# Kernel optimization log

Hardware: AMD Instinct MI355X
Metric: run time of the kernel (lower is better)

Reference implementation:

```python
import jax, jax.numpy as jnp
import numpy as np

THETA = 40.0


def setup_inputs() -> dict:
    key = jax.random.key(0)
    k1, k2 = jax.random.split(key)
    B, C, H, W = 4, 19, 192, 192
    mask = jax.random.normal(k1, (B, C, H, W), dtype=jnp.float32)
    edge = jax.random.uniform(k2, (B, 1, H, W), dtype=jnp.float32)
    return {"mask": mask, "edge": edge, "iter": 3}


def _criss_cross_attention(edge):
    # edge: [B,1,H,W] -> attention logits over K = H + W - 1 criss-cross positions
    e = jax.nn.relu(edge)
    max_edge = e.max()
    hc = jnp.cumsum(e, axis=2)[:, 0]  # [B,H,W] column integral image
    wc = jnp.cumsum(e, axis=3)[:, 0]  # [B,H,W] row integral image
    B, H, W = hc.shape
    # column part: weight[b,t,i,j] = |hc[b,t,j] - hc[b,i,j]|, t in [0,H)
    w_col = jnp.abs(hc[:, :, None, :] - hc[:, None, :, :])  # [B,H,H,W] (b,t,i,j)
    # row part over all columns s: |wc[b,i,s] - wc[b,i,j]|
    wct = wc.transpose(0, 2, 1)  # [B,W(s),H(i)]
    w_row_full = jnp.abs(wct[:, :, :, None] - wc[:, None, :, :])  # [B,W,H,W] (b,s,i,j)
    # drop s == j (self column, already counted in column part): W-1 entries
    t = jnp.arange(W - 1)[:, None]
    j = jnp.arange(W)[None, :]
    idx = t + (t >= j).astype(t.dtype)  # [W-1, W]: source column for slot t at pixel column j
    w_row = jnp.take_along_axis(w_row_full, idx[None, :, None, :], axis=1)  # [B,W-1,H,W]
    logits = -THETA * (jnp.concatenate([w_col, w_row], axis=1) - max_edge)  # [B,H+W-1,H,W]
    attn = jax.nn.softmax(logits, axis=1)
    a_col = attn[:, :H]  # [B,H,H,W]
    a_row = attn[:, H:]  # [B,W-1,H,W]
    # scatter row attention back to full [B,W,H,W] (zero at s==j) for a dense einsum
    attn_full = jnp.zeros((B, W, H, W), attn.dtype).at[:, idx, :, j].set(
        a_row.transpose(1, 3, 0, 2)
    )
    return a_col, attn_full


def reference(mask, edge, iter):
    a_col, a_row_full = _criss_cross_attention(edge)
    feat = mask  # [B,C,H,W]
    for _ in range(iter):
        out_c = jnp.einsum('btij,bctj->bcij', a_col, feat)       # column gather
        out_r = jnp.einsum('bsij,bcis->bcij', a_row_full, feat)  # row gather
        feat = out_c + out_r
    return feat
```

## Files before the change

### kernel.cpp

```cpp
#include <hip/hip_runtime.h>

#define B 4
#define C 19
#define H 192
#define W 192
#define HW (H * W)
#define THETA_LOG2E 57.70780163555855f

#define CSEGS 8
#define CSR 24
#define NCOLB (B * C * 3)
#define NROWB (B * C * H / 8)
#define NTHR 512

__device__ __forceinline__ unsigned short f2b(float x) {
    unsigned u = __float_as_uint(x);
    u = (u + 0x7FFFu + ((u >> 16) & 1u)) >> 16;
    return (unsigned short)u;
}
__device__ __forceinline__ float b2f(unsigned short h) {
    return __uint_as_float(((unsigned)h) << 16);
}

template<bool FIRST>
__global__ __launch_bounds__(NTHR) void k_iter(const float* __restrict__ mask,
                                               const float* __restrict__ edge,
                                               const unsigned short* __restrict__ csin,
                                               const unsigned short* __restrict__ rsin,
                                               unsigned short* __restrict__ csout,
                                               unsigned short* __restrict__ rsout,
                                               float* __restrict__ dcol,
                                               float* __restrict__ drow) {
    const int t = threadIdx.x;
    if (blockIdx.x < NCOLB) {
        __shared__ float sPf[CSEGS * 64], sQf[CSEGS * 64], sPb[CSEGS * 64], sQb[CSEGS * 64];
        int blk = blockIdx.x;
        int jt = blk % 3, bc = blk / 3, b = bc / C, c = bc % C;
        int jl = t & 63, seg = t >> 6;
        int j = jt * 64 + jl, i0 = seg * CSR;

        const float* ep = edge + ((size_t)b * H + i0) * W + j;
        const size_t fb = ((size_t)bc * H + i0) * W + j;
        const size_t db = ((size_t)b * H + i0) * W + j;

        float dr[CSR + 1], fr[CSR];
        #pragma unroll
        for (int r = 0; r < CSR; ++r) dr[r] = exp2f(-THETA_LOG2E * fmaxf(ep[r * W], 0.f));
        dr[CSR] = (seg < CSEGS - 1) ? exp2f(-THETA_LOG2E * fmaxf(ep[CSR * W], 0.f)) : 0.f;

        if (FIRST) {
            #pragma unroll
            for (int r = 0; r < CSR; ++r) fr[r] = mask[fb + r * W];
        } else {
            #pragma unroll
            for (int r = 0; r < CSR; ++r) {
                float cs = b2f(csin[fb + r * W]);
                float rs = b2f(rsin[fb + r * W]);
                float rd = 1.f / (dcol[db + r * W] + drow[db + r * W] - 1.f);
                fr[r] = (cs + rs) * rd;
            }
        }

        float Pf = 1.f, Qf = 0.f, Pb = 1.f, Qb = 0.f;
        #pragma unroll
        for (int r = 0; r < CSR; ++r) { Qf = Qf * dr[r] + fr[r]; Pf *= dr[r]; }
        #pragma unroll
        for (int r = CSR - 1; r >= 0; --r) { Qb = Qb * dr[r + 1] + fr[r]; Pb *= dr[r + 1]; }
        sPf[seg * 64 + jl] = Pf; sQf[seg * 64 + jl] = Qf;
        sPb[seg * 64 + jl] = Pb; sQb[seg * 64 + jl] = Qb;
        __syncthreads();
        if (seg == 0) {
            float P = sPf[jl], Q = sQf[jl];
            for (int s2 = 1; s2 < CSEGS; ++s2) {
                float Pc = sPf[s2 * 64 + jl], Qc = sQf[s2 * 64 + jl];
                Q = Q * Pc + Qc; P = P * Pc;
                sPf[s2 * 64 + jl] = P; sQf[s2 * 64 + jl] = Q;
            }
        } else if (seg == 1) {
            float P = sPb[(CSEGS - 1) * 64 + jl], Q = sQb[(CSEGS - 1) * 64 + jl];
            for (int s2 = CSEGS - 2; s2 >= 0; --s2) {
                float Pc = sPb[s2 * 64 + jl], Qc = sQb[s2 * 64 + jl];
                Q = Q * Pc + Qc; P = P * Pc;
                sPb[s2 * 64 + jl] = P; sQb[s2 * 64 + jl] = Q;
            }
        }
        __syncthreads();
        float z = (seg > 0) ? sQf[(seg - 1) * 64 + jl] : 0.f;
        float s = (seg < CSEGS - 1) ? sQb[(seg + 1) * 64 + jl] : 0.f;
        float zarr[CSR];
        #pragma unroll
        for (int r = 0; r < CSR; ++r) { z = z * dr[r] + fr[r]; zarr[r] = z; }
        #pragma unroll
        for (int r = CSR - 1; r >= 0; --r) {
            s = s * dr[r + 1] + fr[r];
            csout[fb + r * W] = f2b(zarr[r] + s - fr[r]);
        }

        if (FIRST && c == 0) {
            float Pf2 = 1.f, Qf2 = 0.f, Pb2 = 1.f, Qb2 = 0.f;
            #pragma unroll
            for (int r = 0; r < CSR; ++r) { Qf2 = Qf2 * dr[r] + 1.f; Pf2 *= dr[r]; }
            #pragma unroll
            for (int r = CSR - 1; r >= 0; --r) { Qb2 = Qb2 * dr[r + 1] + 1.f; Pb2 *= dr[r + 1]; }
            __syncthreads();
            sPf[seg * 64 + jl] = Pf2; sQf[seg * 64 + jl] = Qf2;
            sPb[seg * 64 + jl] = Pb2; sQb[seg * 64 + jl] = Qb2;
            __syncthreads();
            if (seg == 0) {
                float P = sPf[jl], Q = sQf[jl];
                for (int s2 = 1; s2 < CSEGS; ++s2) {
                    float Pc = sPf[s2 * 64 + jl], Qc = sQf[s2 * 64 + jl];
                    Q = Q * Pc + Qc; P = P * Pc;
                    sPf[s2 * 64 + jl] = P; sQf[s2 * 64 + jl] = Q;
                }
            } else if (seg == 1) {
                float P = sPb[(CSEGS - 1) * 64 + jl], Q = sQb[(CSEGS - 1) * 64 + jl];
                for (int s2 = CSEGS - 2; s2 >= 0; --s2) {
                    float Pc = sPb[s2 * 64 + jl], Qc = sQb[s2 * 64 + jl];
                    Q = Q * Pc + Qc; P = P * Pc;
                    sPb[s2 * 64 + jl] = P; sQb[s2 * 64 + jl] = Q;
                }
            }
            __syncthreads();
            float zu = (seg > 0) ? sQf[(seg - 1) * 64 + jl] : 0.f;
            float su = (seg < CSEGS - 1) ? sQb[(seg + 1) * 64 + jl] : 0.f;
            #pragma unroll
            for (int r = 0; r < CSR; ++r) { zu = zu * dr[r] + 1.f; zarr[r] = zu; }
            #pragma unroll
            for (int r = CSR - 1; r >= 0; --r) {
                su = su * dr[r + 1] + 1.f;
                dcol[db + r * W] = zarr[r] + su - 1.f;
            }
        }
    } else {
        int rblk = blockIdx.x - NCOLB;
        int wave = t >> 6, lane = t & 63;
        int rr = rblk * 8 + wave;
        int i = rr % H;
        int c = (rr / H) % C;
        int b = rr / (H * C);
        const size_t rb = ((size_t)(b * C + c) * H + i) * W;
        const int db = (b * H + i) * W;
        const int s0 = 3 * lane;

        float e0 = edge[db + s0], e1 = edge[db + s0 + 1], e2 = edge[db + s0 + 2];
        float d0 = exp2f(-THETA_LOG2E * fmaxf(e0, 0.f));
        float d1 = exp2f(-THETA_LOG2E * fmaxf(e1, 0.f));
        float d2 = exp2f(-THETA_LOG2E * fmaxf(e2, 0.f));
        float d3 = 0.f;
        if (lane < 63) {
            float e3 = edge[db + s0 + 3];
            d3 = exp2f(-THETA_LOG2E * fmaxf(e3, 0.f));
        }

        float f0, f1, f2;
        if (FIRST) {
            f0 = mask[rb + s0]; f1 = mask[rb + s0 + 1]; f2 = mask[rb + s0 + 2];
        } else {
            float rd0 = 1.f / (dcol[db + s0]     + drow[db + s0]     - 1.f);
            float rd1 = 1.f / (dcol[db + s0 + 1] + drow[db + s0 + 1] - 1.f);
            float rd2 = 1.f / (dcol[db + s0 + 2] + drow[db + s0 + 2] - 1.f);
            f0 = (b2f(csin[rb + s0])     + b2f(rsin[rb + s0]))     * rd0;
            f1 = (b2f(csin[rb + s0 + 1]) + b2f(rsin[rb + s0 + 1])) * rd1;
            f2 = (b2f(csin[rb + s0 + 2]) + b2f(rsin[rb + s0 + 2])) * rd2;
        }

        float P = d0 * d1 * d2;
        float Q = (f0 * d1 + f1) * d2 + f2;
        #pragma unroll
        for (int off = 1; off < 64; off <<= 1) {
            float Pp = __shfl_up(P, off);
            float Qp = __shfl_up(Q, off);
            if (lane >= off) { Q = Qp * P + Q; P = Pp * P; }
        }
        float zin = __shfl_up(Q, 1);
        if (lane == 0) zin = 0.f;
        float zA = zin * d0 + f0;
        float zB = zA * d1 + f1;
        float zC = zB * d2 + f2;

        float Pb = d3 * d2 * d1;
        float Qb = (f2 * d2 + f1) * d1 + f0;
        #pragma unroll
        for (int off = 1; off < 64; off <<= 1) {
            float Pp = __shfl_down(Pb, off);
            float Qp = __shfl_down(Qb, off);
            if (lane < 64 - off) { Qb = Qp * Pb + Qb; Pb = Pp * Pb; }
        }
        float sin_ = __shfl_down(Qb, 1);
        if (lane == 63) sin_ = 0.f;
        float sC = sin_ * d3 + f2;
        float sB = sC * d2 + f1;
        float sA = sB * d1 + f0;

        rsout[rb + s0]     = f2b(zA + sA - 2.f * f0);
        rsout[rb + s0 + 1] = f2b(zB + sB - 2.f * f1);
        rsout[rb + s0 + 2] = f2b(zC + sC - 2.f * f2);

        if (FIRST && c == 0) {
            float Pu = d0 * d1 * d2;
            float Qu = d1 * d2 + d2 + 1.f;
            #pragma unroll
            for (int off = 1; off < 64; off <<= 1) {
                float Pp = __shfl_up(Pu, off);
                float Qp = __shfl_up(Qu, off);
                if (lane >= off) { Qu = Qp * Pu + Qu; Pu = Pp * Pu; }
            }
            float zuin = __shfl_up(Qu, 1);
            if (lane == 0) zuin = 0.f;
            float zuA = zuin * d0 + 1.f;
            float zuB = zuA * d1 + 1.f;
            float zuC = zuB * d2 + 1.f;

            float Pub = d3 * d2 * d1;
            float Qub = d2 * d1 + d1 + 1.f;
            #pragma unroll
            for (int off = 1; off < 64; off <<= 1) {
                float Pp = __shfl_down(Pub, off);
                float Qp = __shfl_down(Qub, off);
                if (lane < 64 - off) { Qub = Qp * Pub + Qub; Pub = Pp * Pub; }
            }
            float suin = __shfl_down(Qub, 1);
            if (lane == 63) suin = 0.f;
            float suC = suin * d3 + 1.f;
            float suB = suC * d2 + 1.f;
            float suA = suB * d1 + 1.f;

            drow[db + s0]     = zuA + suA - 1.f;
            drow[db + s0 + 1] = zuB + suB - 1.f;
            drow[db + s0 + 2] = zuC + suC - 1.f;
        }
    }
}

__global__ __launch_bounds__(256) void k_comb(const unsigned short* __restrict__ cs,
                                              const unsigned short* __restrict__ rs,
                                              const float* __restrict__ dcol,
                                              const float* __restrict__ drow,
                                              float* __restrict__ out) {
    int idx4 = (blockIdx.x * 256 + threadIdx.x) * 4;
    int bc = idx4 / HW;
    int rem = idx4 - bc * HW;
    int b = bc / C;
    size_t db = (size_t)b * HW + rem;
    uint2 csu = *(const uint2*)(cs + idx4);
    uint2 rsu = *(const uint2*)(rs + idx4);
    float4 dc = *(const float4*)(dcol + db);
    float4 dw = *(const float4*)(drow + db);
    float4 o;
    o.x = (b2f((unsigned short)(csu.x & 0xffff)) + b2f((unsigned short)(rsu.x & 0xffff))) / (dc.x + dw.x - 1.f);
    o.y = (b2f((unsigned short)(csu.x >> 16))    + b2f((unsigned short)(rsu.x >> 16)))    / (dc.y + dw.y - 1.f);
    o.z = (b2f((unsigned short)(csu.y & 0xffff)) + b2f((unsigned short)(rsu.y & 0xffff))) / (dc.z + dw.z - 1.f);
    o.w = (b2f((unsigned short)(csu.y >> 16))    + b2f((unsigned short)(rsu.y >> 16)))    / (dc.w + dw.w - 1.f);
    *(float4*)(out + idx4) = o;
}

extern "C" void kernel_launch(void* const* d_in, const int* in_sizes, int n_in,
                              void* d_out, int out_size, void* d_ws, size_t ws_size,
                              hipStream_t stream) {
    const float* mask = (const float*)d_in[0];
    const float* edge = (const float*)d_in[1];
    float* out = (float*)d_out;

    float* dcol = (float*)d_ws;
    float* drow = dcol + (size_t)B * HW;
    unsigned short* csA = (unsigned short*)(drow + (size_t)B * HW);
    unsigned short* rsA = csA + (size_t)B * C * HW;
    unsigned short* csB = rsA + (size_t)B * C * HW;
    unsigned short* rsB = csB + (size_t)B * C * HW;

    const int grid = NCOLB + NROWB;

    k_iter<true><<<grid, NTHR, 0, stream>>>(mask, edge, nullptr, nullptr, csA, rsA, dcol, drow);
    k_iter<false><<<grid, NTHR, 0, stream>>>(nullptr, edge, csA, rsA, csB, rsB, dcol, drow);
    k_iter<false><<<grid, NTHR, 0, stream>>>(nullptr, edge, csB, rsB, csA, rsA, dcol, drow);
    k_comb<<<(B * C * HW) / (4 * 256), 256, 0, stream>>>(csA, rsA, dcol, drow, out);
}
```

Baseline: 50.91 us.

## Cache reciprocal normaliser across iterations and double block size

The second iteration now stores the reciprocal of the normaliser (dcol + drow - 1), written once per batch by the c==0 column blocks. The third iteration and the combine kernel read that single cached array instead of loading dcol and drow and dividing, which removes one float stream and a divide per pixel on those paths. Separately, column segments grow from 8 to 16, with 12 rows each, and blocks go from 512 to 1024 threads, with the row branch handling 16 rows per block. The larger blocks trade a shorter per-thread serial scan for a longer cross-segment scan and possibly lower scheduling flexibility.

```diff
diff --git a/kernel.cpp b/kernel.cpp
--- a/kernel.cpp
+++ b/kernel.cpp
@@ -7,11 +7,11 @@
 #define HW (H * W)
 #define THETA_LOG2E 57.70780163555855f
 
-#define CSEGS 8
-#define CSR 24
+#define CSEGS 16
+#define CSR 12
 #define NCOLB (B * C * 3)
-#define NROWB (B * C * H / 8)
-#define NTHR 512
+#define NROWB (B * C * H / 16)
+#define NTHR 1024
 
 __device__ __forceinline__ unsigned short f2b(float x) {
     unsigned u = __float_as_uint(x);
@@ -22,7 +22,7 @@
     return __uint_as_float(((unsigned)h) << 16);
 }
 
-template<bool FIRST>
+template<int MODE>
 __global__ __launch_bounds__(NTHR) void k_iter(const float* __restrict__ mask,
                                                const float* __restrict__ edge,
                                                const unsigned short* __restrict__ csin,
@@ -30,7 +30,8 @@
                                                unsigned short* __restrict__ csout,
                                                unsigned short* __restrict__ rsout,
                                                float* __restrict__ dcol,
-                                               float* __restrict__ drow) {
+                                               float* __restrict__ drow,
+                                               float* __restrict__ rDg) {
     const int t = threadIdx.x;
     if (blockIdx.x < NCOLB) {
         __shared__ float sPf[CSEGS * 64], sQf[CSEGS * 64], sPb[CSEGS * 64], sQb[CSEGS * 64];
@@ -48,16 +49,24 @@
         for (int r = 0; r < CSR; ++r) dr[r] = exp2f(-THETA_LOG2E * fmaxf(ep[r * W], 0.f));
         dr[CSR] = (seg < CSEGS - 1) ? exp2f(-THETA_LOG2E * fmaxf(ep[CSR * W], 0.f)) : 0.f;
 
-        if (FIRST) {
+        if (MODE == 0) {
             #pragma unroll
             for (int r = 0; r < CSR; ++r) fr[r] = mask[fb + r * W];
-        } else {
+        } else if (MODE == 1) {
             #pragma unroll
             for (int r = 0; r < CSR; ++r) {
                 float cs = b2f(csin[fb + r * W]);
                 float rs = b2f(rsin[fb + r * W]);
                 float rd = 1.f / (dcol[db + r * W] + drow[db + r * W] - 1.f);
                 fr[r] = (cs + rs) * rd;
+                if (c == 0) rDg[db + r * W] = rd;
+            }
+        } else {
+            #pragma unroll
+            for (int r = 0; r < CSR; ++r) {
+                float cs = b2f(csin[fb + r * W]);
+                float rs = b2f(rsin[fb + r * W]);
+                fr[r] = (cs + rs) * rDg[db + r * W];
             }
         }
 
@@ -96,7 +105,7 @@
             csout[fb + r * W] = f2b(zarr[r] + s - fr[r]);
         }
 
-        if (FIRST && c == 0) {
+        if (MODE == 0 && c == 0) {
             float Pf2 = 1.f, Qf2 = 0.f, Pb2 = 1.f, Qb2 = 0.f;
             #pragma unroll
             for (int r = 0; r < CSR; ++r) { Qf2 = Qf2 * dr[r] + 1.f; Pf2 *= dr[r]; }
@@ -135,7 +144,7 @@
     } else {
         int rblk = blockIdx.x - NCOLB;
         int wave = t >> 6, lane = t & 63;
-        int rr = rblk * 8 + wave;
+        int rr = rblk * 16 + wave;
         int i = rr % H;
         int c = (rr / H) % C;
         int b = rr / (H * C);
@@ -154,15 +163,19 @@
         }
 
         float f0, f1, f2;
-        if (FIRST) {
+        if (MODE == 0) {
             f0 = mask[rb + s0]; f1 = mask[rb + s0 + 1]; f2 = mask[rb + s0 + 2];
-        } else {
+        } else if (MODE == 1) {
             float rd0 = 1.f / (dcol[db + s0]     + drow[db + s0]     - 1.f);
             float rd1 = 1.f / (dcol[db + s0 + 1] + drow[db + s0 + 1] - 1.f);
             float rd2 = 1.f / (dcol[db + s0 + 2] + drow[db + s0 + 2] - 1.f);
             f0 = (b2f(csin[rb + s0])     + b2f(rsin[rb + s0]))     * rd0;
             f1 = (b2f(csin[rb + s0 + 1]) + b2f(rsin[rb + s0 + 1])) * rd1;
             f2 = (b2f(csin[rb + s0 + 2]) + b2f(rsin[rb + s0 + 2])) * rd2;
+        } else {
+            f0 = (b2f(csin[rb + s0])     + b2f(rsin[rb + s0]))     * rDg[db + s0];
+            f1 = (b2f(csin[rb + s0 + 1]) + b2f(rsin[rb + s0 + 1])) * rDg[db + s0 + 1];
+            f2 = (b2f(csin[rb + s0 + 2]) + b2f(rsin[rb + s0 + 2])) * rDg[db + s0 + 2];
         }
 
         float P = d0 * d1 * d2;
@@ -197,7 +210,7 @@
         rsout[rb + s0 + 1] = f2b(zB + sB - 2.f * f1);
         rsout[rb + s0 + 2] = f2b(zC + sC - 2.f * f2);
 
-        if (FIRST && c == 0) {
+        if (MODE == 0 && c == 0) {
             float Pu = d0 * d1 * d2;
             float Qu = d1 * d2 + d2 + 1.f;
             #pragma unroll
@@ -235,8 +248,7 @@
 
 __global__ __launch_bounds__(256) void k_comb(const unsigned short* __restrict__ cs,
                                               const unsigned short* __restrict__ rs,
-                                              const float* __restrict__ dcol,
-                                              const float* __restrict__ drow,
+                                              const float* __restrict__ rDg,
                                               float* __restrict__ out) {
     int idx4 = (blockIdx.x * 256 + threadIdx.x) * 4;
     int bc = idx4 / HW;
@@ -245,13 +257,12 @@
     size_t db = (size_t)b * HW + rem;
     uint2 csu = *(const uint2*)(cs + idx4);
     uint2 rsu = *(const uint2*)(rs + idx4);
-    float4 dc = *(const float4*)(dcol + db);
-    float4 dw = *(const float4*)(drow + db);
+    float4 rd = *(const float4*)(rDg + db);
     float4 o;
-    o.x = (b2f((unsigned short)(csu.x & 0xffff)) + b2f((unsigned short)(rsu.x & 0xffff))) / (dc.x + dw.x - 1.f);
-    o.y = (b2f((unsigned short)(csu.x >> 16))    + b2f((unsigned short)(rsu.x >> 16)))    / (dc.y + dw.y - 1.f);
-    o.z = (b2f((unsigned short)(csu.y & 0xffff)) + b2f((unsigned short)(rsu.y & 0xffff))) / (dc.z + dw.z - 1.f);
-    o.w = (b2f((unsigned short)(csu.y >> 16))    + b2f((unsigned short)(rsu.y >> 16)))    / (dc.w + dw.w - 1.f);
+    o.x = (b2f((unsigned short)(csu.x & 0xffff)) + b2f((unsigned short)(rsu.x & 0xffff))) * rd.x;
+    o.y = (b2f((unsigned short)(csu.x >> 16))    + b2f((unsigned short)(rsu.x >> 16)))    * rd.y;
+    o.z = (b2f((unsigned short)(csu.y & 0xffff)) + b2f((unsigned short)(rsu.y & 0xffff))) * rd.z;
+    o.w = (b2f((unsigned short)(csu.y >> 16))    + b2f((unsigned short)(rsu.y >> 16)))    * rd.w;
     *(float4*)(out + idx4) = o;
 }
 
@@ -264,15 +275,16 @@
 
     float* dcol = (float*)d_ws;
     float* drow = dcol + (size_t)B * HW;
-    unsigned short* csA = (unsigned short*)(drow + (size_t)B * HW);
+    float* rDg  = drow + (size_t)B * HW;
+    unsigned short* csA = (unsigned short*)(rDg + (size_t)B * HW);
     unsigned short* rsA = csA + (size_t)B * C * HW;
     unsigned short* csB = rsA + (size_t)B * C * HW;
     unsigned short* rsB = csB + (size_t)B * C * HW;
 
     const int grid = NCOLB + NROWB;
 
-    k_iter<true><<<grid, NTHR, 0, stream>>>(mask, edge, nullptr, nullptr, csA, rsA, dcol, drow);
-    k_iter<false><<<grid, NTHR, 0, stream>>>(nullptr, edge, csA, rsA, csB, rsB, dcol, drow);
-    k_iter<false><<<grid, NTHR, 0, stream>>>(nullptr, edge, csB, rsB, csA, rsA, dcol, drow);
-    k_comb<<<(B * C * HW) / (4 * 256), 256, 0, stream>>>(csA, rsA, dcol, drow, out);
-}
+    k_iter<0><<<grid, NTHR, 0, stream>>>(mask, edge, nullptr, nullptr, csA, rsA, dcol, drow, nullptr);
+    k_iter<1><<<grid, NTHR, 0, stream>>>(nullptr, edge, csA, rsA, csB, rsB, dcol, drow, rDg);
+    k_iter<2><<<grid, NTHR, 0, stream>>>(nullptr, edge, csB, rsB, csA, rsA, nullptr, nullptr, rDg);
+    k_comb<<<(B * C * HW) / (4 * 256), 256, 0, stream>>>(csA, rsA, rDg, out);
+}
```

New measurement: 51.59 us. No clear change (+1.3%).

## Transpose column scans through shared memory and precompute transposed decay/denominator tables

Applied to the files above, without the earlier changes.

Column blocks now stage a full 192x64 tile of the column-sum input in LDS, then run each column as a single-wave shuffle-based linear-recurrence scan. This replaces the 8-segment register scan with its cross-segment shared-memory combine. The first kernel gets dedicated blocks that precompute transposed decay and normalizer tables (dT, dcolT, drowT) plus the normal-layout ones, so later iterations read them contiguously. Row blocks now each process two rows per wave. The change trades extra workspace and a larger LDS footprint, which may lower occupancy, for coalesced scans and less recomputation of exp2.

```diff
diff --git a/kernel.cpp b/kernel.cpp
--- a/kernel.cpp
+++ b/kernel.cpp
@@ -5,13 +5,17 @@
 #define H 192
 #define W 192
 #define HW (H * W)
+#define NP (B * C)
 #define THETA_LOG2E 57.70780163555855f
 
-#define CSEGS 8
-#define CSR 24
-#define NCOLB (B * C * 3)
-#define NROWB (B * C * H / 8)
-#define NTHR 512
+#define NCOL 228
+#define NROW 912
+#define RSTRIDE 7296
+
+#define C1_BEG (NCOL + NROW)
+#define C2_BEG (C1_BEG + 144)
+#define C3_BEG (C2_BEG + 12)
+#define NFIRST (C3_BEG + 12)
 
 __device__ __forceinline__ unsigned short f2b(float x) {
     unsigned u = __float_as_uint(x);
@@ -22,231 +26,271 @@
     return __uint_as_float(((unsigned)h) << 16);
 }
 
-template<bool FIRST>
-__global__ __launch_bounds__(NTHR) void k_iter(const float* __restrict__ mask,
+__device__ __forceinline__ void ks_scan(int lane, float f0, float f1, float f2v,
+                                        float d0, float d1, float d2, float d3,
+                                        float& zA, float& zB, float& zC,
+                                        float& sA, float& sB, float& sC) {
+    float P = d0 * d1 * d2;
+    float Q = (f0 * d1 + f1) * d2 + f2v;
+    #pragma unroll
+    for (int off = 1; off < 64; off <<= 1) {
+        float Pp = __shfl_up(P, off), Qp = __shfl_up(Q, off);
+        if (lane >= off) { Q = Qp * P + Q; P = Pp * P; }
+    }
+    float zin = __shfl_up(Q, 1);
+    if (lane == 0) zin = 0.f;
+    zA = zin * d0 + f0; zB = zA * d1 + f1; zC = zB * d2 + f2v;
+    float Pb = d3 * d2 * d1;
+    float Qb = (f2v * d2 + f1) * d1 + f0;
+    #pragma unroll
+    for (int off = 1; off < 64; off <<= 1) {
+        float Pp = __shfl_down(Pb, off), Qp = __shfl_down(Qb, off);
+        if (lane < 64 - off) { Qb = Qp * Pb + Qb; Pb = Pp * Pb; }
+    }
+    float sin_ = __shfl_down(Qb, 1);
+    if (lane == 63) sin_ = 0.f;
+    sC = sin_ * d3 + f2v; sB = sC * d2 + f1; sA = sB * d1 + f0;
+}
+
+__global__ __launch_bounds__(512) void k_first(const float* __restrict__ mask,
                                                const float* __restrict__ edge,
-                                               const unsigned short* __restrict__ csin,
+                                               unsigned short* __restrict__ csA,
+                                               unsigned short* __restrict__ rsA,
+                                               float* __restrict__ dT,
+                                               float* __restrict__ dcolN,
+                                               float* __restrict__ drowN,
+                                               float* __restrict__ dcolT,
+                                               float* __restrict__ drowT) {
+    __shared__ float tf[192 * 65];
+    __shared__ unsigned short tu[192 * 66];
+    const int t = threadIdx.x, lane = t & 63, wave = t >> 6;
+    const int bx = blockIdx.x;
+
+    if (bx < NCOL) {
+        int jt = bx % 3, p = bx / 3, b = p / C;
+        #pragma unroll
+        for (int k = 0; k < 12; ++k) {
+            int e = t + k * 512; int i = e >> 5, jp = e & 31;
+            float2 mv = *(const float2*)&mask[(size_t)p * HW + i * W + jt * 64 + 2 * jp];
+            ((unsigned*)tu)[33 * i + jp] = (unsigned)f2b(mv.x) | ((unsigned)f2b(mv.y) << 16);
+            float2 ev = *(const float2*)&edge[(size_t)b * HW + i * W + jt * 64 + 2 * jp];
+            tf[65 * i + 2 * jp]     = exp2f(-THETA_LOG2E * fmaxf(ev.x, 0.f));
+            tf[65 * i + 2 * jp + 1] = exp2f(-THETA_LOG2E * fmaxf(ev.y, 0.f));
+        }
+        __syncthreads();
+        #pragma unroll
+        for (int q = 0; q < 8; ++q) {
+            int jl = wave * 8 + q;
+            int r0 = 3 * lane;
+            float f0 = b2f(tu[r0 * 66 + jl]), f1 = b2f(tu[(r0 + 1) * 66 + jl]), f2v = b2f(tu[(r0 + 2) * 66 + jl]);
+            float d0 = tf[r0 * 65 + jl], d1 = tf[(r0 + 1) * 65 + jl], d2 = tf[(r0 + 2) * 65 + jl];
+            float d3 = (lane < 63) ? tf[(r0 + 3) * 65 + jl] : 0.f;
+            float zA, zB, zC, sA, sB, sC;
+            ks_scan(lane, f0, f1, f2v, d0, d1, d2, d3, zA, zB, zC, sA, sB, sC);
+            tu[r0 * 66 + jl]       = f2b(zA + sA - f0);
+            tu[(r0 + 1) * 66 + jl] = f2b(zB + sB - f1);
+            tu[(r0 + 2) * 66 + jl] = f2b(zC + sC - f2v);
+        }
+        __syncthreads();
+        #pragma unroll
+        for (int k = 0; k < 12; ++k) {
+            int e = t + k * 512; int i = e >> 5, jp = e & 31;
+            *(unsigned*)&csA[(size_t)p * HW + i * W + jt * 64 + 2 * jp] = ((unsigned*)tu)[33 * i + jp];
+        }
+    } else if (bx < NCOL + NROW) {
+        int rblk = bx - NCOL;
+        #pragma unroll
+        for (int k = 0; k < 2; ++k) {
+            int rr = rblk * 8 + wave + k * RSTRIDE;
+            int i = rr % H, c = (rr / H) % C, b = rr / (H * C);
+            size_t rb = (size_t)(b * C + c) * HW + (size_t)i * W;
+            size_t db = (size_t)b * HW + (size_t)i * W;
+            int s0 = 3 * lane;
+            float d0 = exp2f(-THETA_LOG2E * fmaxf(edge[db + s0], 0.f));
+            float d1 = exp2f(-THETA_LOG2E * fmaxf(edge[db + s0 + 1], 0.f));
+            float d2 = exp2f(-THETA_LOG2E * fmaxf(edge[db + s0 + 2], 0.f));
+            float d3 = 0.f;
+            if (lane < 63) d3 = exp2f(-THETA_LOG2E * fmaxf(edge[db + s0 + 3], 0.f));
+            float f0 = mask[rb + s0], f1 = mask[rb + s0 + 1], f2v = mask[rb + s0 + 2];
+            float zA, zB, zC, sA, sB, sC;
+            ks_scan(lane, f0, f1, f2v, d0, d1, d2, d3, zA, zB, zC, sA, sB, sC);
+            rsA[rb + s0]     = f2b(zA + sA - 2.f * f0);
+            rsA[rb + s0 + 1] = f2b(zB + sB - 2.f * f1);
+            rsA[rb + s0 + 2] = f2b(zC + sC - 2.f * f2v);
+        }
+    } else if (bx < C2_BEG) {
+        int blk = bx - C1_BEG;
+        int tx = blk % 6, ty = (blk / 6) % 6, b = blk / 36;
+        if (t < 256) {
+            int lx = t % 32, ly = t / 32;
+            #pragma unroll
+            for (int k = 0; k < 4; ++k) {
+                int il = ly + k * 8;
+                int I = ty * 32 + il, J = tx * 32 + lx;
+                float e = edge[(b * H + I) * W + J];
+                tf[il * 33 + lx] = exp2f(-THETA_LOG2E * fmaxf(e, 0.f));
+            }
+        }
+        __syncthreads();
+        if (t < 256) {
+            int lx = t % 32, ly = t / 32;
+            #pragma unroll
+            for (int k = 0; k < 4; ++k) {
+                int jl = ly + k * 8;
+                dT[((size_t)b * W + tx * 32 + jl) * H + ty * 32 + lx] = tf[lx * 33 + jl];
+            }
+        }
+    } else if (bx < C3_BEG) {
+        int bb = bx - C2_BEG; int jt = bb % 3, b = bb / 3;
+        #pragma unroll
+        for (int k = 0; k < 12; ++k) {
+            int e = t + k * 512; int i = e >> 5, jp = e & 31;
+            float2 ev = *(const float2*)&edge[(size_t)b * HW + i * W + jt * 64 + 2 * jp];
+            tf[65 * i + 2 * jp]     = exp2f(-THETA_LOG2E * fmaxf(ev.x, 0.f));
+            tf[65 * i + 2 * jp + 1] = exp2f(-THETA_LOG2E * fmaxf(ev.y, 0.f));
+        }
+        __syncthreads();
+        #pragma unroll
+        for (int q = 0; q < 8; ++q) {
+            int jl = wave * 8 + q;
+            int j = jt * 64 + jl;
+            int r0 = 3 * lane;
+            float d0 = tf[r0 * 65 + jl], d1 = tf[(r0 + 1) * 65 + jl], d2 = tf[(r0 + 2) * 65 + jl];
+            float d3 = (lane < 63) ? tf[(r0 + 3) * 65 + jl] : 0.f;
+            float zA, zB, zC, sA, sB, sC;
+            ks_scan(lane, 1.f, 1.f, 1.f, d0, d1, d2, d3, zA, zB, zC, sA, sB, sC);
+            float uA = zA + sA - 1.f, uB = zB + sB - 1.f, uC = zC + sC - 1.f;
+            size_t tb = ((size_t)b * W + j) * H + r0;
+            dcolT[tb] = uA; dcolT[tb + 1] = uB; dcolT[tb + 2] = uC;
+            tf[r0 * 65 + jl] = uA; tf[(r0 + 1) * 65 + jl] = uB; tf[(r0 + 2) * 65 + jl] = uC;
+        }
+        __syncthreads();
+        #pragma unroll
+        for (int k = 0; k < 24; ++k) {
+            int e = t + k * 512; int i = e >> 6, jl = e & 63;
+            dcolN[(size_t)b * HW + i * W + jt * 64 + jl] = tf[65 * i + jl];
+        }
+    } else {
+        int bb = bx - C3_BEG; int b = bb / 3, i0 = (bb % 3) * 64;
+        #pragma unroll
+        for (int k = 0; k < 8; ++k) {
+            int il = wave * 8 + k;
+            int i = i0 + il;
+            size_t db = (size_t)b * HW + (size_t)i * W;
+            int s0 = 3 * lane;
+            float d0 = exp2f(-THETA_LOG2E * fmaxf(edge[db + s0], 0.f));
+            float d1 = exp2f(-THETA_LOG2E * fmaxf(edge[db + s0 + 1], 0.f));
+            float d2 = exp2f(-THETA_LOG2E * fmaxf(edge[db + s0 + 2], 0.f));
+            float d3 = 0.f;
+            if (lane < 63) d3 = exp2f(-THETA_LOG2E * fmaxf(edge[db + s0 + 3], 0.f));
+            float zA, zB, zC, sA, sB, sC;
+            ks_scan(lane, 1.f, 1.f, 1.f, d0, d1, d2, d3, zA, zB, zC, sA, sB, sC);
+            float uA = zA + sA - 1.f, uB = zB + sB - 1.f, uC = zC + sC - 1.f;
+            drowN[db + s0] = uA; drowN[db + s0 + 1] = uB; drowN[db + s0 + 2] = uC;
+            tf[il * 193 + s0] = uA; tf[il * 193 + s0 + 1] = uB; tf[il * 193 + s0 + 2] = uC;
+        }
+        __syncthreads();
+        #pragma unroll
+        for (int k = 0; k < 24; ++k) {
+            int e = t + k * 512; int j = e >> 6, il = e & 63;
+            drowT[((size_t)b * W + j) * H + i0 + il] = tf[il * 193 + j];
+        }
+    }
+}
+
+__global__ __launch_bounds__(512) void k_iter2(const unsigned short* __restrict__ csin,
                                                const unsigned short* __restrict__ rsin,
                                                unsigned short* __restrict__ csout,
                                                unsigned short* __restrict__ rsout,
-                                               float* __restrict__ dcol,
-                                               float* __restrict__ drow) {
-    const int t = threadIdx.x;
-    if (blockIdx.x < NCOLB) {
-        __shared__ float sPf[CSEGS * 64], sQf[CSEGS * 64], sPb[CSEGS * 64], sQb[CSEGS * 64];
-        int blk = blockIdx.x;
-        int jt = blk % 3, bc = blk / 3, b = bc / C, c = bc % C;
-        int jl = t & 63, seg = t >> 6;
-        int j = jt * 64 + jl, i0 = seg * CSR;
-
-        const float* ep = edge + ((size_t)b * H + i0) * W + j;
-        const size_t fb = ((size_t)bc * H + i0) * W + j;
-        const size_t db = ((size_t)b * H + i0) * W + j;
-
-        float dr[CSR + 1], fr[CSR];
-        #pragma unroll
-        for (int r = 0; r < CSR; ++r) dr[r] = exp2f(-THETA_LOG2E * fmaxf(ep[r * W], 0.f));
-        dr[CSR] = (seg < CSEGS - 1) ? exp2f(-THETA_LOG2E * fmaxf(ep[CSR * W], 0.f)) : 0.f;
-
-        if (FIRST) {
-            #pragma unroll
-            for (int r = 0; r < CSR; ++r) fr[r] = mask[fb + r * W];
-        } else {
-            #pragma unroll
-            for (int r = 0; r < CSR; ++r) {
-                float cs = b2f(csin[fb + r * W]);
-                float rs = b2f(rsin[fb + r * W]);
-                float rd = 1.f / (dcol[db + r * W] + drow[db + r * W] - 1.f);
-                fr[r] = (cs + rs) * rd;
-            }
-        }
-
-        float Pf = 1.f, Qf = 0.f, Pb = 1.f, Qb = 0.f;
-        #pragma unroll
-        for (int r = 0; r < CSR; ++r) { Qf = Qf * dr[r] + fr[r]; Pf *= dr[r]; }
-        #pragma unroll
-        for (int r = CSR - 1; r >= 0; --r) { Qb = Qb * dr[r + 1] + fr[r]; Pb *= dr[r + 1]; }
-        sPf[seg * 64 + jl] = Pf; sQf[seg * 64 + jl] = Qf;
-        sPb[seg * 64 + jl] = Pb; sQb[seg * 64 + jl] = Qb;
-        __syncthreads();
-        if (seg == 0) {
-            float P = sPf[jl], Q = sQf[jl];
-            for (int s2 = 1; s2 < CSEGS; ++s2) {
-                float Pc = sPf[s2 * 64 + jl], Qc = sQf[s2 * 64 + jl];
-                Q = Q * Pc + Qc; P = P * Pc;
-                sPf[s2 * 64 + jl] = P; sQf[s2 * 64 + jl] = Q;
-            }
-        } else if (seg == 1) {
-            float P = sPb[(CSEGS - 1) * 64 + jl], Q = sQb[(CSEGS - 1) * 64 + jl];
-            for (int s2 = CSEGS - 2; s2 >= 0; --s2) {
-                float Pc = sPb[s2 * 64 + jl], Qc = sQb[s2 * 64 + jl];
-                Q = Q * Pc + Qc; P = P * Pc;
-                sPb[s2 * 64 + jl] = P; sQb[s2 * 64 + jl] = Q;
-            }
-        }
-        __syncthreads();
-        float z = (seg > 0) ? sQf[(seg - 1) * 64 + jl] : 0.f;
-        float s = (seg < CSEGS - 1) ? sQb[(seg + 1) * 64 + jl] : 0.f;
-        float zarr[CSR];
-        #pragma unroll
-        for (int r = 0; r < CSR; ++r) { z = z * dr[r] + fr[r]; zarr[r] = z; }
-        #pragma unroll
-        for (int r = CSR - 1; r >= 0; --r) {
-            s = s * dr[r + 1] + fr[r];
-            csout[fb + r * W] = f2b(zarr[r] + s - fr[r]);
-        }
-
-        if (FIRST && c == 0) {
-            float Pf2 = 1.f, Qf2 = 0.f, Pb2 = 1.f, Qb2 = 0.f;
-            #pragma unroll
-            for (int r = 0; r < CSR; ++r) { Qf2 = Qf2 * dr[r] + 1.f; Pf2 *= dr[r]; }
-            #pragma unroll
-            for (int r = CSR - 1; r >= 0; --r) { Qb2 = Qb2 * dr[r + 1] + 1.f; Pb2 *= dr[r + 1]; }
-            __syncthreads();
-            sPf[seg * 64 + jl] = Pf2; sQf[seg * 64 + jl] = Qf2;
-            sPb[seg * 64 + jl] = Pb2; sQb[seg * 64 + jl] = Qb2;
-            __syncthreads();
-            if (seg == 0) {
-                float P = sPf[jl], Q = sQf[jl];
-                for (int s2 = 1; s2 < CSEGS; ++s2) {
-                    float Pc = sPf[s2 * 64 + jl], Qc = sQf[s2 * 64 + jl];
-                    Q = Q * Pc + Qc; P = P * Pc;
-                    sPf[s2 * 64 + jl] = P; sQf[s2 * 64 + jl] = Q;
-                }
-            } else if (seg == 1) {
-                float P = sPb[(CSEGS - 1) * 64 + jl], Q = sQb[(CSEGS - 1) * 64 + jl];
-                for (int s2 = CSEGS - 2; s2 >= 0; --s2) {
-                    float Pc = sPb[s2 * 64 + jl], Qc = sQb[s2 * 64 + jl];
-                    Q = Q * Pc + Qc; P = P * Pc;
-                    sPb[s2 * 64 + jl] = P; sQb[s2 * 64 + jl] = Q;
-                }
-            }
-            __syncthreads();
-            float zu = (seg > 0) ? sQf[(seg - 1) * 64 + jl] : 0.f;
-            float su = (seg < CSEGS - 1) ? sQb[(seg + 1) * 64 + jl] : 0.f;
-            #pragma unroll
-            for (int r = 0; r < CSR; ++r) { zu = zu * dr[r] + 1.f; zarr[r] = zu; }
-            #pragma unroll
-            for (int r = CSR - 1; r >= 0; --r) {
-                su = su * dr[r + 1] + 1.f;
-                dcol[db + r * W] = zarr[r] + su - 1.f;
-            }
+                                               const float* __restrict__ edge,
+                                               const float* __restrict__ dT,
+                                               const float* __restrict__ dcolN,
+                                               const float* __restrict__ drowN,
+                                               const float* __restrict__ dcolT,
+                                               const float* __restrict__ drowT) {
+    __shared__ unsigned short tcs[192 * 66], trs[192 * 66];
+    const int t = threadIdx.x, lane = t & 63, wave = t >> 6;
+    const int bx = blockIdx.x;
+
+    if (bx < NCOL) {
+        int jt = bx % 3, p = bx / 3, b = p / C;
+        #pragma unroll
+        for (int k = 0; k < 12; ++k) {
+            int e = t + k * 512; int i = e >> 5, jp = e & 31;
+            size_t g = (size_t)p * HW + i * W + jt * 64 + 2 * jp;
+            ((unsigned*)tcs)[33 * i + jp] = *(const unsigned*)&csin[g];
+            ((unsigned*)trs)[33 * i + jp] = *(const unsigned*)&rsin[g];
+        }
+        __syncthreads();
+        #pragma unroll
+        for (int q = 0; q < 8; ++q) {
+            int jl = wave * 8 + q;
+            int j = jt * 64 + jl;
+            int r0 = 3 * lane;
+            size_t tb = ((size_t)b * W + j) * H + r0;
+            float rd0 = 1.f / (dcolT[tb]     + drowT[tb]     - 1.f);
+            float rd1 = 1.f / (dcolT[tb + 1] + drowT[tb + 1] - 1.f);
+            float rd2 = 1.f / (dcolT[tb + 2] + drowT[tb + 2] - 1.f);
+            float f0 = (b2f(tcs[r0 * 66 + jl])       + b2f(trs[r0 * 66 + jl]))       * rd0;
+            float f1 = (b2f(tcs[(r0 + 1) * 66 + jl]) + b2f(trs[(r0 + 1) * 66 + jl])) * rd1;
+            float f2v = (b2f(tcs[(r0 + 2) * 66 + jl]) + b2f(trs[(r0 + 2) * 66 + jl])) * rd2;
+            float d0 = dT[tb], d1 = dT[tb + 1], d2 = dT[tb + 2];
+            float d3 = (lane < 63) ? dT[tb + 3] : 0.f;
+            float zA, zB, zC, sA, sB, sC;
+            ks_scan(lane, f0, f1, f2v, d0, d1, d2, d3, zA, zB, zC, sA, sB, sC);
+            tcs[r0 * 66 + jl]       = f2b(zA + sA - f0);
+            tcs[(r0 + 1) * 66 + jl] = f2b(zB + sB - f1);
+            tcs[(r0 + 2) * 66 + jl] = f2b(zC + sC - f2v);
+        }
+        __syncthreads();
+        #pragma unroll
+        for (int k = 0; k < 12; ++k) {
+            int e = t + k * 512; int i = e >> 5, jp = e & 31;
+            *(unsigned*)&csout[(size_t)p * HW + i * W + jt * 64 + 2 * jp] = ((unsigned*)tcs)[33 * i + jp];
         }
     } else {
-        int rblk = blockIdx.x - NCOLB;
-        int wave = t >> 6, lane = t & 63;
-        int rr = rblk * 8 + wave;
-        int i = rr % H;
-        int c = (rr / H) % C;
-        int b = rr / (H * C);
-        const size_t rb = ((size_t)(b * C + c) * H + i) * W;
-        const int db = (b * H + i) * W;
-        const int s0 = 3 * lane;
-
-        float e0 = edge[db + s0], e1 = edge[db + s0 + 1], e2 = edge[db + s0 + 2];
-        float d0 = exp2f(-THETA_LOG2E * fmaxf(e0, 0.f));
-        float d1 = exp2f(-THETA_LOG2E * fmaxf(e1, 0.f));
-        float d2 = exp2f(-THETA_LOG2E * fmaxf(e2, 0.f));
-        float d3 = 0.f;
-        if (lane < 63) {
-            float e3 = edge[db + s0 + 3];
-            d3 = exp2f(-THETA_LOG2E * fmaxf(e3, 0.f));
-        }
-
-        float f0, f1, f2;
-        if (FIRST) {
-            f0 = mask[rb + s0]; f1 = mask[rb + s0 + 1]; f2 = mask[rb + s0 + 2];
-        } else {
-            float rd0 = 1.f / (dcol[db + s0]     + drow[db + s0]     - 1.f);
-            float rd1 = 1.f / (dcol[db + s0 + 1] + drow[db + s0 + 1] - 1.f);
-            float rd2 = 1.f / (dcol[db + s0 + 2] + drow[db + s0 + 2] - 1.f);
-            f0 = (b2f(csin[rb + s0])     + b2f(rsin[rb + s0]))     * rd0;
-            f1 = (b2f(csin[rb + s0 + 1]) + b2f(rsin[rb + s0 + 1])) * rd1;
-            f2 = (b2f(csin[rb + s0 + 2]) + b2f(rsin[rb + s0 + 2])) * rd2;
-        }
-
-        float P = d0 * d1 * d2;
-        float Q = (f0 * d1 + f1) * d2 + f2;
-        #pragma unroll
-        for (int off = 1; off < 64; off <<= 1) {
-            float Pp = __shfl_up(P, off);
-            float Qp = __shfl_up(Q, off);
-            if (lane >= off) { Q = Qp * P + Q; P = Pp * P; }
-        }
-        float zin = __shfl_up(Q, 1);
-        if (lane == 0) zin = 0.f;
-        float zA = zin * d0 + f0;
-        float zB = zA * d1 + f1;
-        float zC = zB * d2 + f2;
-
-        float Pb = d3 * d2 * d1;
-        float Qb = (f2 * d2 + f1) * d1 + f0;
-        #pragma unroll
-        for (int off = 1; off < 64; off <<= 1) {
-            float Pp = __shfl_down(Pb, off);
-            float Qp = __shfl_down(Qb, off);
-            if (lane < 64 - off) { Qb = Qp * Pb + Qb; Pb = Pp * Pb; }
-        }
-        float sin_ = __shfl_down(Qb, 1);
-        if (lane == 63) sin_ = 0.f;
-        float sC = sin_ * d3 + f2;
-        float sB = sC * d2 + f1;
-        float sA = sB * d1 + f0;
-
-        rsout[rb + s0]     = f2b(zA + sA - 2.f * f0);
-        rsout[rb + s0 + 1] = f2b(zB + sB - 2.f * f1);
-        rsout[rb + s0 + 2] = f2b(zC + sC - 2.f * f2);
-
-        if (FIRST && c == 0) {
-            float Pu = d0 * d1 * d2;
-            float Qu = d1 * d2 + d2 + 1.f;
-            #pragma unroll
-            for (int off = 1; off < 64; off <<= 1) {
-                float Pp = __shfl_up(Pu, off);
-                float Qp = __shfl_up(Qu, off);
-                if (lane >= off) { Qu = Qp * Pu + Qu; Pu = Pp * Pu; }
-            }
-            float zuin = __shfl_up(Qu, 1);
-            if (lane == 0) zuin = 0.f;
-            float zuA = zuin * d0 + 1.f;
-            float zuB = zuA * d1 + 1.f;
-            float zuC = zuB * d2 + 1.f;
-
-            float Pub = d3 * d2 * d1;
-            float Qub = d2 * d1 + d1 + 1.f;
-            #pragma unroll
-            for (int off = 1; off < 64; off <<= 1) {
-                float Pp = __shfl_down(Pub, off);
-                float Qp = __shfl_down(Qub, off);
-                if (lane < 64 - off) { Qub = Qp * Pub + Qub; Pub = Pp * Pub; }
-            }
-            float suin = __shfl_down(Qub, 1);
-            if (lane == 63) suin = 0.f;
-            float suC = suin * d3 + 1.f;
-            float suB = suC * d2 + 1.f;
-            float suA = suB * d1 + 1.f;
-
-            drow[db + s0]     = zuA + suA - 1.f;
-            drow[db + s0 + 1] = zuB + suB - 1.f;
-            drow[db + s0 + 2] = zuC + suC - 1.f;
+        int rblk = bx - NCOL;
+        #pragma unroll
+        for (int k = 0; k < 2; ++k) {
+            int rr = rblk * 8 + wave + k * RSTRIDE;
+            int i = rr % H, c = (rr / H) % C, b = rr / (H * C);
+            size_t rb = (size_t)(b * C + c) * HW + (size_t)i * W;
+            size_t db = (size_t)b * HW + (size_t)i * W;
+            int s0 = 3 * lane;
+            float d0 = exp2f(-THETA_LOG2E * fmaxf(edge[db + s0], 0.f));
+            float d1 = exp2f(-THETA_LOG2E * fmaxf(edge[db + s0 + 1], 0.f));
+            float d2 = exp2f(-THETA_LOG2E * fmaxf(edge[db + s0 + 2], 0.f));
+            float d3 = 0.f;
+            if (lane < 63) d3 = exp2f(-THETA_LOG2E * fmaxf(edge[db + s0 + 3], 0.f));
+            float rd0 = 1.f / (dcolN[db + s0]     + drowN[db + s0]     - 1.f);
+            float rd1 = 1.f / (dcolN[db + s0 + 1] + drowN[db + s0 + 1] - 1.f);
+            float rd2 = 1.f / (dcolN[db + s0 + 2] + drowN[db + s0 + 2] - 1.f);
+            float f0 = (b2f(csin[rb + s0])     + b2f(rsin[rb + s0]))     * rd0;
+            float f1 = (b2f(csin[rb + s0 + 1]) + b2f(rsin[rb + s0 + 1])) * rd1;
+            float f2v = (b2f(csin[rb + s0 + 2]) + b2f(rsin[rb + s0 + 2])) * rd2;
+            float zA, zB, zC, sA, sB, sC;
+            ks_scan(lane, f0, f1, f2v, d0, d1, d2, d3, zA, zB, zC, sA, sB, sC);
+            rsout[rb + s0]     = f2b(zA + sA - 2.f * f0);
+            rsout[rb + s0 + 1] = f2b(zB + sB - 2.f * f1);
+            rsout[rb + s0 + 2] = f2b(zC + sC - 2.f * f2v);
         }
     }
 }
 
 __global__ __launch_bounds__(256) void k_comb(const unsigned short* __restrict__ cs,
                                               const unsigned short* __restrict__ rs,
-                                              const float* __restrict__ dcol,
-                                              const float* __restrict__ drow,
+                                              const float* __restrict__ dcolN,
+                                              const float* __restrict__ drowN,
                                               float* __restrict__ out) {
     int idx4 = (blockIdx.x * 256 + threadIdx.x) * 4;
-    int bc = idx4 / HW;
-    int rem = idx4 - bc * HW;
-    int b = bc / C;
+    int p = idx4 / HW;
+    int rem = idx4 - p * HW;
+    int b = p / C;
     size_t db = (size_t)b * HW + rem;
     uint2 csu = *(const uint2*)(cs + idx4);
     uint2 rsu = *(const uint2*)(rs + idx4);
-    float4 dc = *(const float4*)(dcol + db);
-    float4 dw = *(const float4*)(drow + db);
+    float4 dc = *(const float4*)(dcolN + db);
+    float4 dw = *(const float4*)(drowN + db);
     float4 o;
     o.x = (b2f((unsigned short)(csu.x & 0xffff)) + b2f((unsigned short)(rsu.x & 0xffff))) / (dc.x + dw.x - 1.f);
     o.y = (b2f((unsigned short)(csu.x >> 16))    + b2f((unsigned short)(rsu.x >> 16)))    / (dc.y + dw.y - 1.f);
@@ -262,17 +306,18 @@
     const float* edge = (const float*)d_in[1];
     float* out = (float*)d_out;
 
-    float* dcol = (float*)d_ws;
-    float* drow = dcol + (size_t)B * HW;
-    unsigned short* csA = (unsigned short*)(drow + (size_t)B * HW);
-    unsigned short* rsA = csA + (size_t)B * C * HW;
-    unsigned short* csB = rsA + (size_t)B * C * HW;
-    unsigned short* rsB = csB + (size_t)B * C * HW;
-
-    const int grid = NCOLB + NROWB;
-
-    k_iter<true><<<grid, NTHR, 0, stream>>>(mask, edge, nullptr, nullptr, csA, rsA, dcol, drow);
-    k_iter<false><<<grid, NTHR, 0, stream>>>(nullptr, edge, csA, rsA, csB, rsB, dcol, drow);
-    k_iter<false><<<grid, NTHR, 0, stream>>>(nullptr, edge, csB, rsB, csA, rsA, dcol, drow);
-    k_comb<<<(B * C * HW) / (4 * 256), 256, 0, stream>>>(csA, rsA, dcol, drow, out);
-}
+    float* dT    = (float*)d_ws;
+    float* dcolN = dT + (size_t)B * HW;
+    float* drowN = dcolN + (size_t)B * HW;
+    float* dcolT = drowN + (size_t)B * HW;
+    float* drowT = dcolT + (size_t)B * HW;
+    unsigned short* csA = (unsigned short*)(drowT + (size_t)B * HW);
+    unsigned short* rsA = csA + (size_t)NP * HW;
+    unsigned short* csB = rsA + (size_t)NP * HW;
+    unsigned short* rsB = csB + (size_t)NP * HW;
+
+    k_first<<<NFIRST, 512, 0, stream>>>(mask, edge, csA, rsA, dT, dcolN, drowN, dcolT, drowT);
+    k_iter2<<<NCOL + NROW, 512, 0, stream>>>(csA, rsA, csB, rsB, edge, dT, dcolN, drowN, dcolT, drowT);
+    k_iter2<<<NCOL + NROW, 512, 0, stream>>>(csB, rsB, csA, rsA, edge, dT, dcolN, drowN, dcolT, drowT);
+    k_comb<<<(NP * HW) / (4 * 256), 256, 0, stream>>>(csA, rsA, dcolN, drowN, out);
+}
```

After: 60.96 us, median of 2. +19.8%, slower.

## Fuse final combine into last iteration via atomics; vectorize row scan to 4 per lane

Applied to the files above, without the earlier changes.

Removes the separate combine kernel: the last iteration scales column and row sums by the normalizer and atomically adds them into the zeroed output. This avoids writing and rereading bf16 intermediates. The row scan now handles 4 elements per lane with float4 and ushort4 accesses, using 48 active lanes. In exchange it adds a memset and float atomics on the output, and a quarter of the lanes in each row wave sit idle.

```diff
diff --git a/kernel.cpp b/kernel.cpp
--- a/kernel.cpp
+++ b/kernel.cpp
@@ -5,6 +5,7 @@
 #define H 192
 #define W 192
 #define HW (H * W)
+#define NP (B * C)
 #define THETA_LOG2E 57.70780163555855f
 
 #define CSEGS 8
@@ -22,7 +23,7 @@
     return __uint_as_float(((unsigned)h) << 16);
 }
 
-template<bool FIRST>
+template<int MODE>
 __global__ __launch_bounds__(NTHR) void k_iter(const float* __restrict__ mask,
                                                const float* __restrict__ edge,
                                                const unsigned short* __restrict__ csin,
@@ -30,7 +31,8 @@
                                                unsigned short* __restrict__ csout,
                                                unsigned short* __restrict__ rsout,
                                                float* __restrict__ dcol,
-                                               float* __restrict__ drow) {
+                                               float* __restrict__ drow,
+                                               float* __restrict__ outg) {
     const int t = threadIdx.x;
     if (blockIdx.x < NCOLB) {
         __shared__ float sPf[CSEGS * 64], sQf[CSEGS * 64], sPb[CSEGS * 64], sQb[CSEGS * 64];
@@ -48,7 +50,7 @@
         for (int r = 0; r < CSR; ++r) dr[r] = exp2f(-THETA_LOG2E * fmaxf(ep[r * W], 0.f));
         dr[CSR] = (seg < CSEGS - 1) ? exp2f(-THETA_LOG2E * fmaxf(ep[CSR * W], 0.f)) : 0.f;
 
-        if (FIRST) {
+        if (MODE == 0) {
             #pragma unroll
             for (int r = 0; r < CSR; ++r) fr[r] = mask[fb + r * W];
         } else {
@@ -90,13 +92,22 @@
         float zarr[CSR];
         #pragma unroll
         for (int r = 0; r < CSR; ++r) { z = z * dr[r] + fr[r]; zarr[r] = z; }
-        #pragma unroll
-        for (int r = CSR - 1; r >= 0; --r) {
-            s = s * dr[r + 1] + fr[r];
-            csout[fb + r * W] = f2b(zarr[r] + s - fr[r]);
-        }
-
-        if (FIRST && c == 0) {
+        if (MODE == 2) {
+            #pragma unroll
+            for (int r = CSR - 1; r >= 0; --r) {
+                s = s * dr[r + 1] + fr[r];
+                float rd = 1.f / (dcol[db + r * W] + drow[db + r * W] - 1.f);
+                atomicAdd(&outg[fb + r * W], (zarr[r] + s - fr[r]) * rd);
+            }
+        } else {
+            #pragma unroll
+            for (int r = CSR - 1; r >= 0; --r) {
+                s = s * dr[r + 1] + fr[r];
+                csout[fb + r * W] = f2b(zarr[r] + s - fr[r]);
+            }
+        }
+
+        if (MODE == 0 && c == 0) {
             float Pf2 = 1.f, Qf2 = 0.f, Pb2 = 1.f, Qb2 = 0.f;
             #pragma unroll
             for (int r = 0; r < CSR; ++r) { Qf2 = Qf2 * dr[r] + 1.f; Pf2 *= dr[r]; }
@@ -140,33 +151,45 @@
         int c = (rr / H) % C;
         int b = rr / (H * C);
         const size_t rb = ((size_t)(b * C + c) * H + i) * W;
-        const int db = (b * H + i) * W;
-        const int s0 = 3 * lane;
-
-        float e0 = edge[db + s0], e1 = edge[db + s0 + 1], e2 = edge[db + s0 + 2];
-        float d0 = exp2f(-THETA_LOG2E * fmaxf(e0, 0.f));
-        float d1 = exp2f(-THETA_LOG2E * fmaxf(e1, 0.f));
-        float d2 = exp2f(-THETA_LOG2E * fmaxf(e2, 0.f));
-        float d3 = 0.f;
-        if (lane < 63) {
-            float e3 = edge[db + s0 + 3];
-            d3 = exp2f(-THETA_LOG2E * fmaxf(e3, 0.f));
-        }
-
-        float f0, f1, f2;
-        if (FIRST) {
-            f0 = mask[rb + s0]; f1 = mask[rb + s0 + 1]; f2 = mask[rb + s0 + 2];
-        } else {
-            float rd0 = 1.f / (dcol[db + s0]     + drow[db + s0]     - 1.f);
-            float rd1 = 1.f / (dcol[db + s0 + 1] + drow[db + s0 + 1] - 1.f);
-            float rd2 = 1.f / (dcol[db + s0 + 2] + drow[db + s0 + 2] - 1.f);
-            f0 = (b2f(csin[rb + s0])     + b2f(rsin[rb + s0]))     * rd0;
-            f1 = (b2f(csin[rb + s0 + 1]) + b2f(rsin[rb + s0 + 1])) * rd1;
-            f2 = (b2f(csin[rb + s0 + 2]) + b2f(rsin[rb + s0 + 2])) * rd2;
-        }
-
-        float P = d0 * d1 * d2;
-        float Q = (f0 * d1 + f1) * d2 + f2;
+        const size_t db = ((size_t)b * H + i) * W;
+        const bool act = lane < 48;
+        const int s0 = 4 * (act ? lane : 47);
+
+        float d0 = 0.f, d1 = 0.f, d2 = 0.f, d3 = 0.f;
+        float f0 = 0.f, f1 = 0.f, f2v = 0.f, f3 = 0.f;
+        float rd0 = 0.f, rd1 = 0.f, rd2 = 0.f, rd3 = 0.f;
+        if (act) {
+            float4 ev = *(const float4*)&edge[db + s0];
+            d0 = exp2f(-THETA_LOG2E * fmaxf(ev.x, 0.f));
+            d1 = exp2f(-THETA_LOG2E * fmaxf(ev.y, 0.f));
+            d2 = exp2f(-THETA_LOG2E * fmaxf(ev.z, 0.f));
+            d3 = exp2f(-THETA_LOG2E * fmaxf(ev.w, 0.f));
+            if (MODE == 0) {
+                float4 mv = *(const float4*)&mask[rb + s0];
+                f0 = mv.x; f1 = mv.y; f2v = mv.z; f3 = mv.w;
+            } else {
+                float4 dc = *(const float4*)&dcol[db + s0];
+                float4 dw = *(const float4*)&drow[db + s0];
+                rd0 = 1.f / (dc.x + dw.x - 1.f);
+                rd1 = 1.f / (dc.y + dw.y - 1.f);
+                rd2 = 1.f / (dc.z + dw.z - 1.f);
+                rd3 = 1.f / (dc.w + dw.w - 1.f);
+                ushort4 cu = *(const ushort4*)&csin[rb + s0];
+                ushort4 ru = *(const ushort4*)&rsin[rb + s0];
+                f0  = (b2f(cu.x) + b2f(ru.x)) * rd0;
+                f1  = (b2f(cu.y) + b2f(ru.y)) * rd1;
+                f2v = (b2f(cu.z) + b2f(ru.z)) * rd2;
+                f3  = (b2f(cu.w) + b2f(ru.w)) * rd3;
+            }
+        }
+        float d4 = __shfl_down(d0, 1);
+        if (lane >= 47) d4 = 0.f;
+
+        float P = 1.f, Q = 0.f;
+        if (act) {
+            P = d0 * d1 * d2 * d3;
+            Q = ((f0 * d1 + f1) * d2 + f2v) * d3 + f3;
+        }
         #pragma unroll
         for (int off = 1; off < 64; off <<= 1) {
             float Pp = __shfl_up(P, off);
@@ -177,10 +200,14 @@
         if (lane == 0) zin = 0.f;
         float zA = zin * d0 + f0;
         float zB = zA * d1 + f1;
-        float zC = zB * d2 + f2;
-
-        float Pb = d3 * d2 * d1;
-        float Qb = (f2 * d2 + f1) * d1 + f0;
+        float zC = zB * d2 + f2v;
+        float zD = zC * d3 + f3;
+
+        float Pb = 1.f, Qb = 0.f;
+        if (act) {
+            Pb = d4 * d3 * d2 * d1;
+            Qb = ((f3 * d3 + f2v) * d2 + f1) * d1 + f0;
+        }
         #pragma unroll
         for (int off = 1; off < 64; off <<= 1) {
             float Pp = __shfl_down(Pb, off);
@@ -189,17 +216,33 @@
         }
         float sin_ = __shfl_down(Qb, 1);
         if (lane == 63) sin_ = 0.f;
-        float sC = sin_ * d3 + f2;
+        float sD = sin_ * d4 + f3;
+        float sC = sD * d3 + f2v;
         float sB = sC * d2 + f1;
         float sA = sB * d1 + f0;
 
-        rsout[rb + s0]     = f2b(zA + sA - 2.f * f0);
-        rsout[rb + s0 + 1] = f2b(zB + sB - 2.f * f1);
-        rsout[rb + s0 + 2] = f2b(zC + sC - 2.f * f2);
-
-        if (FIRST && c == 0) {
-            float Pu = d0 * d1 * d2;
-            float Qu = d1 * d2 + d2 + 1.f;
+        if (act) {
+            if (MODE == 2) {
+                atomicAdd(&outg[rb + s0],     (zA + sA - 2.f * f0)  * rd0);
+                atomicAdd(&outg[rb + s0 + 1], (zB + sB - 2.f * f1)  * rd1);
+                atomicAdd(&outg[rb + s0 + 2], (zC + sC - 2.f * f2v) * rd2);
+                atomicAdd(&outg[rb + s0 + 3], (zD + sD - 2.f * f3)  * rd3);
+            } else {
+                ushort4 o;
+                o.x = f2b(zA + sA - 2.f * f0);
+                o.y = f2b(zB + sB - 2.f * f1);
+                o.z = f2b(zC + sC - 2.f * f2v);
+                o.w = f2b(zD + sD - 2.f * f3);
+                *(ushort4*)&rsout[rb + s0] = o;
+            }
+        }
+
+        if (MODE == 0 && c == 0) {
+            float Pu = 1.f, Qu = 0.f;
+            if (act) {
+                Pu = d0 * d1 * d2 * d3;
+                Qu = ((d1 + 1.f) * d2 + 1.f) * d3 + 1.f;
+            }
             #pragma unroll
             for (int off = 1; off < 64; off <<= 1) {
                 float Pp = __shfl_up(Pu, off);
@@ -211,9 +254,13 @@
             float zuA = zuin * d0 + 1.f;
             float zuB = zuA * d1 + 1.f;
             float zuC = zuB * d2 + 1.f;
-
-            float Pub = d3 * d2 * d1;
-            float Qub = d2 * d1 + d1 + 1.f;
+            float zuD = zuC * d3 + 1.f;
+
+            float Pub = 1.f, Qub = 0.f;
+            if (act) {
+                Pub = d4 * d3 * d2 * d1;
+                Qub = ((d3 + 1.f) * d2 + 1.f) * d1 + 1.f;
+            }
             #pragma unroll
             for (int off = 1; off < 64; off <<= 1) {
                 float Pp = __shfl_down(Pub, off);
@@ -222,37 +269,21 @@
             }
             float suin = __shfl_down(Qub, 1);
             if (lane == 63) suin = 0.f;
-            float suC = suin * d3 + 1.f;
+            float suD = suin * d4 + 1.f;
+            float suC = suD * d3 + 1.f;
             float suB = suC * d2 + 1.f;
             float suA = suB * d1 + 1.f;
 
-            drow[db + s0]     = zuA + suA - 1.f;
-            drow[db + s0 + 1] = zuB + suB - 1.f;
-            drow[db + s0 + 2] = zuC + suC - 1.f;
+            if (act) {
+                float4 o;
+                o.x = zuA + suA - 1.f;
+                o.y = zuB + suB - 1.f;
+                o.z = zuC + suC - 1.f;
+                o.w = zuD + suD - 1.f;
+                *(float4*)&drow[db + s0] = o;
+            }
         }
     }
-}
-
-__global__ __launch_bounds__(256) void k_comb(const unsigned short* __restrict__ cs,
-                                              const unsigned short* __restrict__ rs,
-                                              const float* __restrict__ dcol,
-                                              const float* __restrict__ drow,
-                                              float* __restrict__ out) {
-    int idx4 = (blockIdx.x * 256 + threadIdx.x) * 4;
-    int bc = idx4 / HW;
-    int rem = idx4 - bc * HW;
-    int b = bc / C;
-    size_t db = (size_t)b * HW + rem;
-    uint2 csu = *(const uint2*)(cs + idx4);
-    uint2 rsu = *(const uint2*)(rs + idx4);
-    float4 dc = *(const float4*)(dcol + db);
-    float4 dw = *(const float4*)(drow + db);
-    float4 o;
-    o.x = (b2f((unsigned short)(csu.x & 0xffff)) + b2f((unsigned short)(rsu.x & 0xffff))) / (dc.x + dw.x - 1.f);
-    o.y = (b2f((unsigned short)(csu.x >> 16))    + b2f((unsigned short)(rsu.x >> 16)))    / (dc.y + dw.y - 1.f);
-    o.z = (b2f((unsigned short)(csu.y & 0xffff)) + b2f((unsigned short)(rsu.y & 0xffff))) / (dc.z + dw.z - 1.f);
-    o.w = (b2f((unsigned short)(csu.y >> 16))    + b2f((unsigned short)(rsu.y >> 16)))    / (dc.w + dw.w - 1.f);
-    *(float4*)(out + idx4) = o;
 }
 
 extern "C" void kernel_launch(void* const* d_in, const int* in_sizes, int n_in,
@@ -265,14 +296,14 @@
     float* dcol = (float*)d_ws;
     float* drow = dcol + (size_t)B * HW;
     unsigned short* csA = (unsigned short*)(drow + (size_t)B * HW);
-    unsigned short* rsA = csA + (size_t)B * C * HW;
-    unsigned short* csB = rsA + (size_t)B * C * HW;
-    unsigned short* rsB = csB + (size_t)B * C * HW;
+    unsigned short* rsA = csA + (size_t)NP * HW;
+    unsigned short* csB = rsA + (size_t)NP * HW;
+    unsigned short* rsB = csB + (size_t)NP * HW;
 
     const int grid = NCOLB + NROWB;
 
-    k_iter<true><<<grid, NTHR, 0, stream>>>(mask, edge, nullptr, nullptr, csA, rsA, dcol, drow);
-    k_iter<false><<<grid, NTHR, 0, stream>>>(nullptr, edge, csA, rsA, csB, rsB, dcol, drow);
-    k_iter<false><<<grid, NTHR, 0, stream>>>(nullptr, edge, csB, rsB, csA, rsA, dcol, drow);
-    k_comb<<<(B * C * HW) / (4 * 256), 256, 0, stream>>>(csA, rsA, dcol, drow, out);
+    hipMemsetAsync(out, 0, (size_t)NP * HW * sizeof(float), stream);
+    k_iter<0><<<grid, NTHR, 0, stream>>>(mask, edge, nullptr, nullptr, csA, rsA, dcol, drow, nullptr);
+    k_iter<1><<<grid, NTHR, 0, stream>>>(nullptr, edge, csA, rsA, csB, rsB, dcol, drow, nullptr);
+    k_iter<2><<<grid, NTHR, 0, stream>>>(nullptr, edge, csB, rsB, nullptr, nullptr, dcol, drow, out);
 }
```

Measured after the change: 87.73 us. +72.3%, slower.
